# Kernel tuning notes

Measured on AMD Instinct MI355X. Metric: run time of the kernel, lower is better.

Reference implementation:

```python
import jax, jax.numpy as jnp
import numpy as np

B, T, N, F, D, E = 8, 256, 118, 3, 128, 372
G = B * T  # number of graphs after flattening batch*time


def _gcn(x, src, dst, W, b):
    # x: [G, N, Fin] -> PyG GCNConv: X' = D^-1/2 (A+I) D^-1/2 (X W) + b
    h = x @ W  # [G, N, Fout]
    deg = jnp.ones((N,), h.dtype).at[dst].add(1.0)  # in-degree + self loop
    inv = deg ** -0.5
    norm = inv[src] * inv[dst]  # [E]
    agg = h * (1.0 / deg)[None, :, None]  # self-loop term: inv[i]*inv[i] = 1/deg
    agg = agg.at[:, dst].add(h[:, src] * norm[None, :, None])
    return agg + b


def _lstm_layer(x, Wih, Whh, bih, bhh):
    # x: [B, T, I]; PyTorch gate order i, f, g, o
    Bb, H = x.shape[0], Whh.shape[1]
    h0 = jnp.zeros((Bb, H), x.dtype)
    c0 = jnp.zeros((Bb, H), x.dtype)

    def step(carry, xt):
        h, c = carry
        gates = xt @ Wih.T + h @ Whh.T + bih + bhh
        i, f, g, o = jnp.split(gates, 4, axis=-1)
        c = jax.nn.sigmoid(f) * c + jax.nn.sigmoid(i) * jnp.tanh(g)
        h = jax.nn.sigmoid(o) * jnp.tanh(c)
        return (h, c), h

    _, ys = jax.lax.scan(step, (h0, c0), jnp.swapaxes(x, 0, 1))
    return jnp.swapaxes(ys, 0, 1)


def setup_inputs() -> dict:
    key = jax.random.key(0)
    ks = jax.random.split(key, 24)
    s = 0.05

    def rn(i, shape):
        return jax.random.normal(ks[i], shape, jnp.float32) * s

    return {
        "snapshot_sequence": jax.random.normal(ks[0], (B, T, N, F), jnp.float32),
        "edge_index": jax.random.randint(ks[1], (2, E), 0, N, dtype=jnp.int64),
        "scale": jnp.ones((F,), jnp.float32),
        "shift": jnp.zeros((F,), jnp.float32),
        "W1": rn(2, (F, D)), "b1": jnp.zeros((D,), jnp.float32),
        "W2": rn(3, (D, D)), "b2": jnp.zeros((D,), jnp.float32),
        "W3": rn(4, (D, D)), "b3": jnp.zeros((D,), jnp.float32),
        "Wih0": rn(5, (4 * D, D)), "Whh0": rn(6, (4 * D, D)),
        "bih0": jnp.zeros((4 * D,), jnp.float32), "bhh0": jnp.zeros((4 * D,), jnp.float32),
        "Wih1": rn(7, (4 * D, D)), "Whh1": rn(8, (4 * D, D)),
        "bih1": jnp.zeros((4 * D,), jnp.float32), "bhh1": jnp.zeros((4 * D,), jnp.float32),
        "hW1": rn(9, (D, 128)), "hb1": jnp.zeros((128,), jnp.float32),
        "hW2": rn(10, (128, 64)), "hb2": jnp.zeros((64,), jnp.float32),
        "hW3": rn(11, (64, 2)), "hb3": jnp.zeros((2,), jnp.float32),
    }


def reference(snapshot_sequence, edge_index, scale, shift,
              W1, b1, W2, b2, W3, b3,
              Wih0, Whh0, bih0, bhh0, Wih1, Whh1, bih1, bhh1,
              hW1, hb1, hW2, hb2, hW3, hb3):
    src, dst = edge_index[0], edge_index[1]
    x = snapshot_sequence * scale + shift              # FeatureNormalizer
    x = x.reshape(G, N, F)                             # flatten batch*time graphs
    x = jax.nn.silu(_gcn(x, src, dst, W1, b1))         # GCNConv 1 (dropout = eval identity)
    x = jax.nn.silu(_gcn(x, src, dst, W2, b2))         # GCNConv 2
    x = jax.nn.silu(_gcn(x, src, dst, W3, b3))         # GCNConv 3
    emb = x.mean(axis=1)                               # global_mean_pool -> [G, D]
    emb = emb.reshape(B, T, D)
    h = _lstm_layer(emb, Wih0, Whh0, bih0, bhh0)       # 2-layer LSTM (eval: no dropout)
    h = _lstm_layer(h, Wih1, Whh1, bih1, bhh1)
    final = h[:, -1, :]                                # [B, D]
    y = jax.nn.silu(final @ hW1 + hb1)
    y = jax.nn.silu(y @ hW2 + hb2)
    y = y @ hW3 + hb3
    return jax.nn.softplus(y) + 1e-6                   # [B, 2]
```

## Files before the change

### kernel.cpp

```cpp
#include <hip/hip_runtime.h>
#include <math.h>

#define NN 118
#define EE 372
#define GG 2048
#define DD 128
#define TT 256
#define BB 8
#define FD 512

#define XS 136

typedef short bf16x8 __attribute__((ext_vector_type(8)));
typedef float f32x4  __attribute__((ext_vector_type(4)));
typedef _Float16 f16x2 __attribute__((ext_vector_type(2)));

__device__ __forceinline__ float frcp_(float x) { return __builtin_amdgcn_rcpf(x); }
__device__ __forceinline__ float sig_f(float x) { return frcp_(1.0f + __expf(-x)); }
__device__ __forceinline__ float tanh_f(float x) { return 1.0f - 2.0f * frcp_(__expf(2.0f * x) + 1.0f); }
__device__ __forceinline__ float silu_f(float x) { return x * frcp_(1.0f + __expf(-x)); }
__device__ __forceinline__ float siluf_(float x) { return x / (1.0f + expf(-x)); }

__device__ __forceinline__ float fdot2_(unsigned int a, unsigned int b, float c) {
#if defined(__has_builtin) && __has_builtin(__builtin_amdgcn_fdot2)
    return __builtin_amdgcn_fdot2(__builtin_bit_cast(f16x2, a),
                                  __builtin_bit_cast(f16x2, b), c, false);
#else
    f16x2 x = __builtin_bit_cast(f16x2, a), y = __builtin_bit_cast(f16x2, b);
    return c + (float)x[0] * (float)y[0] + (float)x[1] * (float)y[1];
#endif
}

__device__ __forceinline__ void bar_lds() {
    asm volatile("s_waitcnt lgkmcnt(0)\n\ts_barrier" ::: "memory");
}

__device__ __forceinline__ unsigned short f2bf(float x) {
    unsigned int u = __float_as_uint(x);
    unsigned int r = (u + 0x7fffu + ((u >> 16) & 1u)) >> 16;
    return (unsigned short)r;
}
__device__ __forceinline__ float bf2f(unsigned short b) {
    return __uint_as_float(((unsigned int)b) << 16);
}

__global__ void prep_kernel(const int* __restrict__ ei,
                            const float* __restrict__ bih0, const float* __restrict__ bhh0,
                            const float* __restrict__ bih1, const float* __restrict__ bhh1,
                            float* __restrict__ bias0, float* __restrict__ bias1,
                            unsigned short* __restrict__ AbG) {
    __shared__ int sflag;
    __shared__ int ssrc[EE], sdst[EE];
    __shared__ int scount[NN];
    __shared__ float sinv[NN];
    __shared__ float Adense[NN * NN];
    int tid = threadIdx.x;
    if (tid == 0) sflag = 0;
    __syncthreads();
    for (int i = tid; i < 2 * EE; i += blockDim.x)
        if ((i & 1) && ei[i] != 0) atomicOr(&sflag, 1);
    __syncthreads();
    bool m64 = (sflag == 0);
    for (int e = tid; e < EE; e += blockDim.x) {
        int s, d;
        if (m64) { s = ei[2 * e]; d = ei[2 * EE + 2 * e]; }
        else     { s = ei[e];     d = ei[EE + e]; }
        s = min(max(s, 0), NN - 1); d = min(max(d, 0), NN - 1);
        ssrc[e] = s; sdst[e] = d;
    }
    for (int n = tid; n < NN; n += blockDim.x) scount[n] = 0;
    for (int i = tid; i < NN * NN; i += blockDim.x) Adense[i] = 0.0f;
    __syncthreads();
    for (int e = tid; e < EE; e += blockDim.x) atomicAdd(&scount[sdst[e]], 1);
    __syncthreads();
    for (int n = tid; n < NN; n += blockDim.x) {
        float deg = 1.0f + (float)scount[n];
        sinv[n] = rsqrtf(deg);
        Adense[n * NN + n] = 1.0f / deg;
    }
    __syncthreads();
    for (int e = tid; e < EE; e += blockDim.x)
        atomicAdd(&Adense[sdst[e] * NN + ssrc[e]], sinv[ssrc[e]] * sinv[sdst[e]]);
    __syncthreads();
    for (int i = tid; i < 128 * 128; i += blockDim.x) {
        int r = i >> 7, c = i & 127;
        AbG[i] = (r < NN && c < NN) ? f2bf(Adense[r * NN + c]) : (unsigned short)0;
    }
    for (int j = tid; j < FD; j += blockDim.x) {
        bias0[j] = bih0[j] + bhh0[j];
        bias1[j] = bih1[j] + bhh1[j];
    }
}

__global__ void convw_kernel(const float* __restrict__ W, unsigned short* __restrict__ out) {
    int i = blockIdx.x * 512 + threadIdx.x;
    int n = i >> 7, k = i & 127;
    out[i] = f2bf(W[k * DD + n]);
}

__global__ void convh_kernel(const float* __restrict__ W, unsigned int* __restrict__ out) {
    int i = blockIdx.x * 512 + threadIdx.x;
    int d = i & 127;
    int rest = i >> 7;
    int quarter = rest & 3;
    int qg = rest >> 2;
    int q = qg & 15, g = qg >> 4;
    const float* row = W + (size_t)(g * 128 + d) * 128 + quarter * 32;
    float a = row[2 * q], b = row[2 * q + 1];
    unsigned short lo = __builtin_bit_cast(unsigned short, (_Float16)a);
    unsigned short hi = __builtin_bit_cast(unsigned short, (_Float16)b);
    out[i] = (unsigned int)lo | ((unsigned int)hi << 16);
}

__global__ void transpose_kernel(const float* __restrict__ in, float* __restrict__ out) {
    int idx = blockIdx.x * blockDim.x + threadIdx.x;
    int j = idx >> 7, k = idx & 127;
    out[k * FD + j] = in[idx];
}

__device__ __forceinline__ void mm_xw(const unsigned short* __restrict__ xb,
                                      const unsigned short* __restrict__ wtG,
                                      unsigned short* __restrict__ hS, int tid) {
    int lane = tid & 63, w = tid >> 6;
    int lm = lane & 15, lq = lane >> 4;
    int wm = (w & 1) * 64, wn = (w >> 1) * 32;
    f32x4 acc[4][2];
#pragma unroll
    for (int mt = 0; mt < 4; ++mt)
#pragma unroll
        for (int nt = 0; nt < 2; ++nt) acc[mt][nt] = (f32x4){0.f, 0.f, 0.f, 0.f};
#pragma unroll
    for (int kb = 0; kb < 4; ++kb) {
        int ko = kb * 32 + lq * 8;
        bf16x8 b0 = *(const bf16x8*)(wtG + (wn + lm) * 128 + ko);
        bf16x8 b1 = *(const bf16x8*)(wtG + (wn + 16 + lm) * 128 + ko);
#pragma unroll
        for (int mt = 0; mt < 4; ++mt) {
            bf16x8 af = *(const bf16x8*)(xb + (wm + mt * 16 + lm) * XS + ko);
            acc[mt][0] = __builtin_amdgcn_mfma_f32_16x16x32_bf16(af, b0, acc[mt][0], 0, 0, 0);
            acc[mt][1] = __builtin_amdgcn_mfma_f32_16x16x32_bf16(af, b1, acc[mt][1], 0, 0, 0);
        }
    }
#pragma unroll
    for (int mt = 0; mt < 4; ++mt)
#pragma unroll
        for (int nt = 0; nt < 2; ++nt) {
            f32x4 a = acc[mt][nt];
            ushort4 pk;
            pk.x = f2bf(a[0]); pk.y = f2bf(a[1]); pk.z = f2bf(a[2]); pk.w = f2bf(a[3]);
            *(ushort4*)(hS + (wn + nt * 16 + lm) * XS + wm + mt * 16 + lq * 4) = pk;
        }
}

__device__ __forceinline__ void mm_agg(const unsigned short* __restrict__ AbG,
                                       const unsigned short* __restrict__ hS,
                                       unsigned short* __restrict__ xb,
                                       float bn0, float bn1, int tid) {
    int lane = tid & 63, w = tid >> 6;
    int lm = lane & 15, lq = lane >> 4;
    int wm = (w & 1) * 64, wn = (w >> 1) * 32;
    f32x4 acc[4][2];
#pragma unroll
    for (int mt = 0; mt < 4; ++mt)
#pragma unroll
        for (int nt = 0; nt < 2; ++nt) acc[mt][nt] = (f32x4){0.f, 0.f, 0.f, 0.f};
#pragma unroll
    for (int kb = 0; kb < 4; ++kb) {
        int ko = kb * 32 + lq * 8;
        bf16x8 b0 = *(const bf16x8*)(hS + (wn + lm) * XS + ko);
        bf16x8 b1 = *(const bf16x8*)(hS + (wn + 16 + lm) * XS + ko);
#pragma unroll
        for (int mt = 0; mt < 4; ++mt) {
            bf16x8 af = *(const bf16x8*)(AbG + (wm + mt * 16 + lm) * 128 + ko);
            acc[mt][0] = __builtin_amdgcn_mfma_f32_16x16x32_bf16(af, b0, acc[mt][0], 0, 0, 0);
            acc[mt][1] = __builtin_amdgcn_mfma_f32_16x16x32_bf16(af, b1, acc[mt][1], 0, 0, 0);
        }
    }
#pragma unroll
    for (int mt = 0; mt < 4; ++mt)
#pragma unroll
        for (int nt = 0; nt < 2; ++nt) {
            float bn = nt ? bn1 : bn0;
            int col = wn + nt * 16 + lm;
#pragma unroll
            for (int i = 0; i < 4; ++i) {
                float v = silu_f(acc[mt][nt][i] + bn);
                xb[(wm + mt * 16 + lq * 4 + i) * XS + col] = f2bf(v);
            }
        }
}

__global__ __launch_bounds__(512) void gcn_kernel(
    const float* __restrict__ xg, const float* __restrict__ scale, const float* __restrict__ shift,
    const float* __restrict__ W1, const float* __restrict__ b1,
    const float* __restrict__ b2, const float* __restrict__ b3,
    const unsigned short* __restrict__ AbG,
    const unsigned short* __restrict__ Wt2g, const unsigned short* __restrict__ Wt3g,
    float* __restrict__ emb) {
    extern __shared__ char smem[];
    unsigned short* xb = (unsigned short*)smem;
    unsigned short* hS = (unsigned short*)(smem + 34816);
    float* xinL  = (float*)(smem + 69632);
    float* meanS = (float*)(smem + 71056);
    int tid = threadIdx.x;
    int lane = tid & 63, w = tid >> 6;
    int g = blockIdx.x;

    for (int i = tid; i < 2176; i += 512) ((uint4*)hS)[i] = (uint4){0, 0, 0, 0};
    for (int i = tid; i < 170; i += 512) ((uint4*)(xb + NN * XS))[i] = (uint4){0, 0, 0, 0};
    float s0 = scale[0], s1 = scale[1], s2 = scale[2];
    float t0 = shift[0], t1 = shift[1], t2 = shift[2];
    const float* xrow = xg + (size_t)g * (NN * 3);
    for (int i = tid; i < NN * 3; i += 512) {
        int f = i % 3;
        float sc = (f == 0) ? s0 : ((f == 1) ? s1 : s2);
        float sf = (f == 0) ? t0 : ((f == 1) ? t1 : t2);
        xinL[i] = xrow[i] * sc + sf;
    }
    int lm = lane & 15;
    int wn = (w >> 1) * 32;
    int n0 = wn + lm, n1 = wn + 16 + lm;
    float b1a = b1[n0], b1b = b1[n1];
    float b2a = b2[n0], b2b = b2[n1];
    float b3a = b3[n0], b3b = b3[n1];
    int dd = lane * 2;
    float2 w10 = *(const float2*)(W1 + dd);
    float2 w11 = *(const float2*)(W1 + DD + dd);
    float2 w12 = *(const float2*)(W1 + 2 * DD + dd);
    bar_lds();
    for (int k = 0; k < 15; ++k) {
        int n = w + 8 * k;
        if (n >= NN) break;
        float x0 = xinL[n * 3], x1 = xinL[n * 3 + 1], x2 = xinL[n * 3 + 2];
        hS[dd * XS + n]       = f2bf(x0 * w10.x + x1 * w11.x + x2 * w12.x);
        hS[(dd + 1) * XS + n] = f2bf(x0 * w10.y + x1 * w11.y + x2 * w12.y);
    }
    bar_lds();
    mm_agg(AbG, hS, xb, b1a, b1b, tid);
    bar_lds();
    mm_xw(xb, Wt2g, hS, tid);
    bar_lds();
    mm_agg(AbG, hS, xb, b2a, b2b, tid);
    bar_lds();
    mm_xw(xb, Wt3g, hS, tid);
    bar_lds();
    mm_agg(AbG, hS, xb, b3a, b3b, tid);
    bar_lds();
    {
        int d = tid & 127, part = tid >> 7;
        int a0 = part * 30;
        int a1 = (a0 + 30 < NN) ? (a0 + 30) : NN;
        float s = 0.f;
        for (int n = a0; n < a1; ++n) s += bf2f(xb[n * XS + d]);
        meanS[part * 128 + d] = s;
    }
    bar_lds();
    if (tid < 128) {
        float s = meanS[tid] + meanS[128 + tid] + meanS[256 + tid] + meanS[384 + tid];
        emb[(size_t)g * DD + tid] = s * (1.0f / (float)NN);
    }
}

__global__ __launch_bounds__(512) void proj_kernel(const float* __restrict__ src,
                                                   const float* __restrict__ WT,
                                                   const float* __restrict__ bias,
                                                   float* __restrict__ dst) {
    __shared__ __align__(16) float eL[DD];
    int g = blockIdx.x, tid = threadIdx.x;
    if (tid < DD) eL[tid] = src[(size_t)g * DD + tid];
    __syncthreads();
    float acc = bias[tid];
    const float* wt = WT + tid;
#pragma unroll 8
    for (int k = 0; k < DD; ++k) acc += eL[k] * wt[(size_t)k * FD];
    dst[(size_t)g * FD + tid] = acc;
}

__global__ __launch_bounds__(512, 2) void scan_kernel(
    const float* __restrict__ inp,
    const unsigned int* __restrict__ Wc,
    float* __restrict__ hout, int full) {
    __shared__ __align__(16) unsigned short hL[DD];
    __shared__ __align__(16) float sgP[3 * DD * 4];
    int b = blockIdx.x, j = threadIdx.x;
    int d = j & 127, quarter = j >> 7;
    unsigned int wreg[4][16];
#pragma unroll
    for (int g = 0; g < 4; ++g)
#pragma unroll
        for (int q = 0; q < 16; ++q)
            wreg[g][q] = Wc[(((g * 16 + q) << 2) + quarter) * 128 + d];
#pragma unroll
    for (int g = 0; g < 4; ++g)
#pragma unroll
        for (int q = 0; q < 16; ++q)
            asm volatile("" : "+v"(wreg[g][q]));
    if (j < 64) ((unsigned int*)hL)[j] = 0u;
    float creg = 0.f;
    const float* ib = inp + (size_t)b * TT * FD;
    float* hb_ = hout + (size_t)b * (full ? TT * DD : DD);
    float xg0[4], xg1[4];
    if (quarter == 0) {
#pragma unroll
        for (int g = 0; g < 4; ++g) { xg0[g] = ib[g * DD + d]; xg1[g] = ib[FD + g * DD + d]; }
    }
    bar_lds();
    for (int t = 0; t < TT; ++t) {
        float xg2[4];
        if (quarter == 0) {
            bool more = (t + 2 < TT);
#pragma unroll
            for (int g = 0; g < 4; ++g)
                xg2[g] = more ? ib[(t + 2) * FD + g * DD + d] : 0.f;
        }
        const uint4* h4 = (const uint4*)(hL + quarter * 32);
        float a0 = 0.f, a1 = 0.f, a2 = 0.f, a3 = 0.f;
#pragma unroll
        for (int c = 0; c < 4; ++c) {
            uint4 hv = h4[c];
            a0 = fdot2_(wreg[0][4 * c + 0], hv.x, a0);
            a1 = fdot2_(wreg[1][4 * c + 0], hv.x, a1);
            a2 = fdot2_(wreg[2][4 * c + 0], hv.x, a2);
            a3 = fdot2_(wreg[3][4 * c + 0], hv.x, a3);
            a0 = fdot2_(wreg[0][4 * c + 1], hv.y, a0);
            a1 = fdot2_(wreg[1][4 * c + 1], hv.y, a1);
            a2 = fdot2_(wreg[2][4 * c + 1], hv.y, a2);
            a3 = fdot2_(wreg[3][4 * c + 1], hv.y, a3);
            a0 = fdot2_(wreg[0][4 * c + 2], hv.z, a0);
            a1 = fdot2_(wreg[1][4 * c + 2], hv.z, a1);
            a2 = fdot2_(wreg[2][4 * c + 2], hv.z, a2);
            a3 = fdot2_(wreg[3][4 * c + 2], hv.z, a3);
            a0 = fdot2_(wreg[0][4 * c + 3], hv.w, a0);
            a1 = fdot2_(wreg[1][4 * c + 3], hv.w, a1);
            a2 = fdot2_(wreg[2][4 * c + 3], hv.w, a2);
            a3 = fdot2_(wreg[3][4 * c + 3], hv.w, a3);
        }
        if (quarter != 0)
            *(float4*)(sgP + ((quarter - 1) * DD + d) * 4) = make_float4(a0, a1, a2, a3);
        bar_lds();
        if (quarter == 0) {
            float4 p1 = *(const float4*)(sgP + d * 4);
            float4 p2 = *(const float4*)(sgP + (DD + d) * 4);
            float4 p3 = *(const float4*)(sgP + (2 * DD + d) * 4);
            float iv = sig_f(a0 + p1.x + p2.x + p3.x + xg0[0]);
            float fv = sig_f(a1 + p1.y + p2.y + p3.y + xg0[1]);
            float gv = tanh_f(a2 + p1.z + p2.z + p3.z + xg0[2]);
            float ov = sig_f(a3 + p1.w + p2.w + p3.w + xg0[3]);
            float cn = fv * creg + iv * gv;
            creg = cn;
            float hn = ov * tanh_f(cn);
            ((_Float16*)hL)[d] = (_Float16)hn;
            if (full) hb_[t * DD + d] = hn;
            else if (t == TT - 1) hb_[d] = hn;
#pragma unroll
            for (int g = 0; g < 4; ++g) { xg0[g] = xg1[g]; xg1[g] = xg2[g]; }
        }
        bar_lds();
    }
}

__global__ void head_kernel(const float* __restrict__ hfin,
                            const float* __restrict__ hW1, const float* __restrict__ hb1,
                            const float* __restrict__ hW2, const float* __restrict__ hb2,
                            const float* __restrict__ hW3, const float* __restrict__ hb3,
                            float* __restrict__ out) {
    __shared__ float fh[BB * DD];
    __shared__ float y1[BB * DD];
    __shared__ float y2[BB * 64];
    int tid = threadIdx.x;
    for (int i = tid; i < BB * DD; i += 256) fh[i] = hfin[i];
    __syncthreads();
    for (int i = tid; i < BB * DD; i += 256) {
        int bb = i >> 7, jj = i & 127;
        float acc = hb1[jj];
        for (int k = 0; k < DD; ++k) acc += fh[(bb << 7) + k] * hW1[(k << 7) + jj];
        y1[i] = siluf_(acc);
    }
    __syncthreads();
    for (int i = tid; i < BB * 64; i += 256) {
        int bb = i >> 6, jj = i & 63;
        float acc = hb2[jj];
        for (int k = 0; k < DD; ++k) acc += y1[(bb << 7) + k] * hW2[(k << 6) + jj];
        y2[i] = siluf_(acc);
    }
    __syncthreads();
    if (tid < BB * 2) {
        int bb = tid >> 1, m = tid & 1;
        float acc = hb3[m];
        for (int k = 0; k < 64; ++k) acc += y2[(bb << 6) + k] * hW3[k * 2 + m];
        float sp = fmaxf(acc, 0.f) + log1pf(expf(-fabsf(acc)));
        out[tid] = sp + 1e-6f;
    }
}

extern "C" void kernel_launch(void* const* d_in, const int* in_sizes, int n_in,
                              void* d_out, int out_size, void* d_ws, size_t ws_size,
                              hipStream_t stream) {
    const float* snap  = (const float*)d_in[0];
    const int*   edges = (const int*)d_in[1];
    const float* scale = (const float*)d_in[2];
    const float* shift = (const float*)d_in[3];
    const float* W1 = (const float*)d_in[4];
    const float* b1 = (const float*)d_in[5];
    const float* W2 = (const float*)d_in[6];
    const float* b2 = (const float*)d_in[7];
    const float* W3 = (const float*)d_in[8];
    const float* b3 = (const float*)d_in[9];
    const float* Wih0 = (const float*)d_in[10];
    const float* Whh0 = (const float*)d_in[11];
    const float* bih0 = (const float*)d_in[12];
    const float* bhh0 = (const float*)d_in[13];
    const float* Wih1 = (const float*)d_in[14];
    const float* Whh1 = (const float*)d_in[15];
    const float* bih1 = (const float*)d_in[16];
    const float* bhh1 = (const float*)d_in[17];
    const float* hW1 = (const float*)d_in[18];
    const float* hb1 = (const float*)d_in[19];
    const float* hW2 = (const float*)d_in[20];
    const float* hb2 = (const float*)d_in[21];
    const float* hW3 = (const float*)d_in[22];
    const float* hb3 = (const float*)d_in[23];

    float* ws = (float*)d_ws;
    float* bias0 = ws + 0;
    float* bias1 = ws + 512;
    unsigned short* AbG  = (unsigned short*)(ws + 1024);
    unsigned short* Wt2g = (unsigned short*)(ws + 9216);
    unsigned short* Wt3g = (unsigned short*)(ws + 17408);
    float* WT0 = ws + 25600;
    float* WT1 = ws + 91136;
    unsigned int* Wc0 = (unsigned int*)(ws + 156672);
    unsigned int* Wc1 = (unsigned int*)(ws + 189440);
    float* emb   = ws + 222208;
    float* inp   = ws + 484352;
    float* h0seq = ws + 1532928;
    float* hfin  = ws + 1795072;

    const int smem_gcn = 73104;
    hipFuncSetAttribute((const void*)gcn_kernel,
                        hipFuncAttributeMaxDynamicSharedMemorySize, smem_gcn);

    prep_kernel<<<1, 256, 0, stream>>>(edges, bih0, bhh0, bih1, bhh1,
                                       bias0, bias1, AbG);
    convw_kernel<<<32, 512, 0, stream>>>(W2, Wt2g);
    convw_kernel<<<32, 512, 0, stream>>>(W3, Wt3g);
    convh_kernel<<<64, 512, 0, stream>>>(Whh0, Wc0);
    convh_kernel<<<64, 512, 0, stream>>>(Whh1, Wc1);
    transpose_kernel<<<128, 512, 0, stream>>>(Wih0, WT0);
    transpose_kernel<<<128, 512, 0, stream>>>(Wih1, WT1);
    gcn_kernel<<<GG, 512, smem_gcn, stream>>>(snap, scale, shift, W1, b1, b2, b3,
                                              AbG, Wt2g, Wt3g, emb);
    proj_kernel<<<GG, 512, 0, stream>>>(emb, WT0, bias0, inp);
    scan_kernel<<<BB, 512, 0, stream>>>(inp, Wc0, h0seq, 1);
    proj_kernel<<<GG, 512, 0, stream>>>(h0seq, WT1, bias1, inp);
    scan_kernel<<<BB, 512, 0, stream>>>(inp, Wc1, hfin, 0);
    head_kernel<<<1, 256, 0, stream>>>(hfin, hW1, hb1, hW2, hb2, hW3, hb3, (float*)d_out);
}
```

Before: 627.1 us.

## Process two graphs per GCN block with larger per-wave MFMA tiles

The GCN kernel now handles two graphs per 512-thread block, four waves per graph. Each wave computes a 64x64 output tile instead of 64x32, so every loaded A fragment feeds four MFMAs instead of two, and the grid is halved. The aim is more operand reuse and less per-block setup and barrier overhead. In exchange, LDS use roughly doubles to about 142KB, likely limiting each CU to one block, and the extra accumulators raise register pressure, which may reduce latency hiding.

```diff
diff --git a/kernel.cpp b/kernel.cpp
--- a/kernel.cpp
+++ b/kernel.cpp
@@ -10,6 +10,7 @@
 #define FD 512
 
 #define XS 136
+#define MS 264
 
 typedef short bf16x8 __attribute__((ext_vector_type(8)));
 typedef float f32x4  __attribute__((ext_vector_type(4)));
@@ -118,79 +119,81 @@
     out[k * FD + j] = in[idx];
 }
 
-__device__ __forceinline__ void mm_xw(const unsigned short* __restrict__ xb,
-                                      const unsigned short* __restrict__ wtG,
-                                      unsigned short* __restrict__ hS, int tid) {
-    int lane = tid & 63, w = tid >> 6;
-    int lm = lane & 15, lq = lane >> 4;
-    int wm = (w & 1) * 64, wn = (w >> 1) * 32;
-    f32x4 acc[4][2];
+__device__ __forceinline__ void mm_agg2(const unsigned short* __restrict__ AbG,
+                                        const unsigned short* __restrict__ hS2,
+                                        unsigned short* __restrict__ xb2,
+                                        const float* __restrict__ bias,
+                                        int gr, int wm, int wn, int lm, int lq) {
+    f32x4 acc[4][4];
 #pragma unroll
     for (int mt = 0; mt < 4; ++mt)
 #pragma unroll
-        for (int nt = 0; nt < 2; ++nt) acc[mt][nt] = (f32x4){0.f, 0.f, 0.f, 0.f};
+        for (int nt = 0; nt < 4; ++nt) acc[mt][nt] = (f32x4){0.f, 0.f, 0.f, 0.f};
 #pragma unroll
     for (int kb = 0; kb < 4; ++kb) {
         int ko = kb * 32 + lq * 8;
-        bf16x8 b0 = *(const bf16x8*)(wtG + (wn + lm) * 128 + ko);
-        bf16x8 b1 = *(const bf16x8*)(wtG + (wn + 16 + lm) * 128 + ko);
+        bf16x8 bfr[4];
+#pragma unroll
+        for (int nt = 0; nt < 4; ++nt)
+            bfr[nt] = *(const bf16x8*)(hS2 + (wn + nt * 16 + lm) * MS + gr * 128 + ko);
 #pragma unroll
         for (int mt = 0; mt < 4; ++mt) {
-            bf16x8 af = *(const bf16x8*)(xb + (wm + mt * 16 + lm) * XS + ko);
-            acc[mt][0] = __builtin_amdgcn_mfma_f32_16x16x32_bf16(af, b0, acc[mt][0], 0, 0, 0);
-            acc[mt][1] = __builtin_amdgcn_mfma_f32_16x16x32_bf16(af, b1, acc[mt][1], 0, 0, 0);
-        }
-    }
+            bf16x8 af = *(const bf16x8*)(AbG + (wm + mt * 16 + lm) * 128 + ko);
+#pragma unroll
+            for (int nt = 0; nt < 4; ++nt)
+                acc[mt][nt] = __builtin_amdgcn_mfma_f32_16x16x32_bf16(af, bfr[nt], acc[mt][nt], 0, 0, 0);
+        }
+    }
+#pragma unroll
+    for (int nt = 0; nt < 4; ++nt) {
+        float bn = bias[wn + nt * 16 + lm];
+        int col = wn + nt * 16 + lm;
+#pragma unroll
+        for (int mt = 0; mt < 4; ++mt)
+#pragma unroll
+            for (int i = 0; i < 4; ++i) {
+                float v = silu_f(acc[mt][nt][i] + bn);
+                xb2[(gr * 128 + wm + mt * 16 + lq * 4 + i) * XS + col] = f2bf(v);
+            }
+    }
+}
+
+__device__ __forceinline__ void mm_xw2(const unsigned short* __restrict__ xb2,
+                                       const unsigned short* __restrict__ WtG,
+                                       unsigned short* __restrict__ hS2,
+                                       int gr, int wm, int wn, int lm, int lq) {
+    f32x4 acc[4][4];
 #pragma unroll
     for (int mt = 0; mt < 4; ++mt)
 #pragma unroll
-        for (int nt = 0; nt < 2; ++nt) {
+        for (int nt = 0; nt < 4; ++nt) acc[mt][nt] = (f32x4){0.f, 0.f, 0.f, 0.f};
+#pragma unroll
+    for (int kb = 0; kb < 4; ++kb) {
+        int ko = kb * 32 + lq * 8;
+        bf16x8 bfr[4];
+#pragma unroll
+        for (int nt = 0; nt < 4; ++nt)
+            bfr[nt] = *(const bf16x8*)(WtG + (wn + nt * 16 + lm) * 128 + ko);
+#pragma unroll
+        for (int mt = 0; mt < 4; ++mt) {
+            bf16x8 af = *(const bf16x8*)(xb2 + (gr * 128 + wm + mt * 16 + lm) * XS + ko);
+#pragma unroll
+            for (int nt = 0; nt < 4; ++nt)
+                acc[mt][nt] = __builtin_amdgcn_mfma_f32_16x16x32_bf16(af, bfr[nt], acc[mt][nt], 0, 0, 0);
+        }
+    }
+#pragma unroll
+    for (int nt = 0; nt < 4; ++nt)
+#pragma unroll
+        for (int mt = 0; mt < 4; ++mt) {
             f32x4 a = acc[mt][nt];
             ushort4 pk;
             pk.x = f2bf(a[0]); pk.y = f2bf(a[1]); pk.z = f2bf(a[2]); pk.w = f2bf(a[3]);
-            *(ushort4*)(hS + (wn + nt * 16 + lm) * XS + wm + mt * 16 + lq * 4) = pk;
-        }
-}
-
-__device__ __forceinline__ void mm_agg(const unsigned short* __restrict__ AbG,
-                                       const unsigned short* __restrict__ hS,
-                                       unsigned short* __restrict__ xb,
-                                       float bn0, float bn1, int tid) {
-    int lane = tid & 63, w = tid >> 6;
-    int lm = lane & 15, lq = lane >> 4;
-    int wm = (w & 1) * 64, wn = (w >> 1) * 32;
-    f32x4 acc[4][2];
-#pragma unroll
-    for (int mt = 0; mt < 4; ++mt)
-#pragma unroll
-        for (int nt = 0; nt < 2; ++nt) acc[mt][nt] = (f32x4){0.f, 0.f, 0.f, 0.f};
-#pragma unroll
-    for (int kb = 0; kb < 4; ++kb) {
-        int ko = kb * 32 + lq * 8;
-        bf16x8 b0 = *(const bf16x8*)(hS + (wn + lm) * XS + ko);
-        bf16x8 b1 = *(const bf16x8*)(hS + (wn + 16 + lm) * XS + ko);
-#pragma unroll
-        for (int mt = 0; mt < 4; ++mt) {
-            bf16x8 af = *(const bf16x8*)(AbG + (wm + mt * 16 + lm) * 128 + ko);
-            acc[mt][0] = __builtin_amdgcn_mfma_f32_16x16x32_bf16(af, b0, acc[mt][0], 0, 0, 0);
-            acc[mt][1] = __builtin_amdgcn_mfma_f32_16x16x32_bf16(af, b1, acc[mt][1], 0, 0, 0);
-        }
-    }
-#pragma unroll
-    for (int mt = 0; mt < 4; ++mt)
-#pragma unroll
-        for (int nt = 0; nt < 2; ++nt) {
-            float bn = nt ? bn1 : bn0;
-            int col = wn + nt * 16 + lm;
-#pragma unroll
-            for (int i = 0; i < 4; ++i) {
-                float v = silu_f(acc[mt][nt][i] + bn);
-                xb[(wm + mt * 16 + lq * 4 + i) * XS + col] = f2bf(v);
-            }
-        }
-}
-
-__global__ __launch_bounds__(512) void gcn_kernel(
+            *(ushort4*)(hS2 + (wn + nt * 16 + lm) * MS + gr * 128 + wm + mt * 16 + lq * 4) = pk;
+        }
+}
+
+__global__ __launch_bounds__(512, 2) void gcn_kernel(
     const float* __restrict__ xg, const float* __restrict__ scale, const float* __restrict__ shift,
     const float* __restrict__ W1, const float* __restrict__ b1,
     const float* __restrict__ b2, const float* __restrict__ b3,
@@ -198,66 +201,72 @@
     const unsigned short* __restrict__ Wt2g, const unsigned short* __restrict__ Wt3g,
     float* __restrict__ emb) {
     extern __shared__ char smem[];
-    unsigned short* xb = (unsigned short*)smem;
-    unsigned short* hS = (unsigned short*)(smem + 34816);
-    float* xinL  = (float*)(smem + 69632);
-    float* meanS = (float*)(smem + 71056);
+    unsigned short* xb2 = (unsigned short*)smem;
+    unsigned short* hS2 = (unsigned short*)(smem + 69632);
+    float* xin2  = (float*)(smem + 137216);
+    float* meanS = (float*)(smem + 140048);
     int tid = threadIdx.x;
     int lane = tid & 63, w = tid >> 6;
-    int g = blockIdx.x;
-
-    for (int i = tid; i < 2176; i += 512) ((uint4*)hS)[i] = (uint4){0, 0, 0, 0};
-    for (int i = tid; i < 170; i += 512) ((uint4*)(xb + NN * XS))[i] = (uint4){0, 0, 0, 0};
+    int gr = w >> 2;
+    int wl = w & 3;
+    int lm = lane & 15, lq = lane >> 4;
+    int wm = (wl & 1) * 64, wn = (wl >> 1) * 64;
+    int g0 = blockIdx.x * 2;
+
+    for (int i = tid; i < 4224; i += 512) ((uint4*)hS2)[i] = (uint4){0, 0, 0, 0};
+    for (int i = tid; i < 2 * 10 * 64; i += 512) {
+        int grr = i >= 640;
+        int ii = i - grr * 640;
+        int r = grr * 128 + NN + (ii >> 6), c = (ii & 63) * 2;
+        *(unsigned int*)(xb2 + r * XS + c) = 0u;
+    }
     float s0 = scale[0], s1 = scale[1], s2 = scale[2];
     float t0 = shift[0], t1 = shift[1], t2 = shift[2];
-    const float* xrow = xg + (size_t)g * (NN * 3);
-    for (int i = tid; i < NN * 3; i += 512) {
-        int f = i % 3;
+    for (int i = tid; i < 2 * NN * 3; i += 512) {
+        int gi = (i >= NN * 3) ? 1 : 0;
+        int idx = i - gi * (NN * 3);
+        int f = idx % 3;
         float sc = (f == 0) ? s0 : ((f == 1) ? s1 : s2);
         float sf = (f == 0) ? t0 : ((f == 1) ? t1 : t2);
-        xinL[i] = xrow[i] * sc + sf;
-    }
-    int lm = lane & 15;
-    int wn = (w >> 1) * 32;
-    int n0 = wn + lm, n1 = wn + 16 + lm;
-    float b1a = b1[n0], b1b = b1[n1];
-    float b2a = b2[n0], b2b = b2[n1];
-    float b3a = b3[n0], b3b = b3[n1];
+        xin2[gi * 354 + idx] = xg[(size_t)(g0 + gi) * (NN * 3) + idx] * sc + sf;
+    }
     int dd = lane * 2;
     float2 w10 = *(const float2*)(W1 + dd);
     float2 w11 = *(const float2*)(W1 + DD + dd);
     float2 w12 = *(const float2*)(W1 + 2 * DD + dd);
     bar_lds();
-    for (int k = 0; k < 15; ++k) {
-        int n = w + 8 * k;
+    const float* xin = xin2 + gr * 354;
+    for (int k = 0; k < 30; ++k) {
+        int n = wl + 4 * k;
         if (n >= NN) break;
-        float x0 = xinL[n * 3], x1 = xinL[n * 3 + 1], x2 = xinL[n * 3 + 2];
-        hS[dd * XS + n]       = f2bf(x0 * w10.x + x1 * w11.x + x2 * w12.x);
-        hS[(dd + 1) * XS + n] = f2bf(x0 * w10.y + x1 * w11.y + x2 * w12.y);
-    }
-    bar_lds();
-    mm_agg(AbG, hS, xb, b1a, b1b, tid);
-    bar_lds();
-    mm_xw(xb, Wt2g, hS, tid);
-    bar_lds();
-    mm_agg(AbG, hS, xb, b2a, b2b, tid);
-    bar_lds();
-    mm_xw(xb, Wt3g, hS, tid);
-    bar_lds();
-    mm_agg(AbG, hS, xb, b3a, b3b, tid);
+        float x0 = xin[n * 3], x1 = xin[n * 3 + 1], x2 = xin[n * 3 + 2];
+        hS2[dd * MS + gr * 128 + n]       = f2bf(x0 * w10.x + x1 * w11.x + x2 * w12.x);
+        hS2[(dd + 1) * MS + gr * 128 + n] = f2bf(x0 * w10.y + x1 * w11.y + x2 * w12.y);
+    }
+    bar_lds();
+    mm_agg2(AbG, hS2, xb2, b1, gr, wm, wn, lm, lq);
+    bar_lds();
+    mm_xw2(xb2, Wt2g, hS2, gr, wm, wn, lm, lq);
+    bar_lds();
+    mm_agg2(AbG, hS2, xb2, b2, gr, wm, wn, lm, lq);
+    bar_lds();
+    mm_xw2(xb2, Wt3g, hS2, gr, wm, wn, lm, lq);
+    bar_lds();
+    mm_agg2(AbG, hS2, xb2, b3, gr, wm, wn, lm, lq);
     bar_lds();
     {
-        int d = tid & 127, part = tid >> 7;
-        int a0 = part * 30;
-        int a1 = (a0 + 30 < NN) ? (a0 + 30) : NN;
+        int grr = tid >> 8, t2 = tid & 255;
+        int part = t2 >> 7, d = t2 & 127;
+        int a0 = part * 59, a1 = a0 + 59;
         float s = 0.f;
-        for (int n = a0; n < a1; ++n) s += bf2f(xb[n * XS + d]);
-        meanS[part * 128 + d] = s;
-    }
-    bar_lds();
-    if (tid < 128) {
-        float s = meanS[tid] + meanS[128 + tid] + meanS[256 + tid] + meanS[384 + tid];
-        emb[(size_t)g * DD + tid] = s * (1.0f / (float)NN);
+        for (int n = a0; n < a1; ++n) s += bf2f(xb2[(grr * 128 + n) * XS + d]);
+        meanS[grr * 256 + part * 128 + d] = s;
+    }
+    bar_lds();
+    if (tid < 256) {
+        int grr = tid >> 7, d = tid & 127;
+        float s = meanS[grr * 256 + d] + meanS[grr * 256 + 128 + d];
+        emb[(size_t)(g0 + grr) * DD + d] = s * (1.0f / (float)NN);
     }
 }
 
@@ -436,7 +445,7 @@
     float* h0seq = ws + 1532928;
     float* hfin  = ws + 1795072;
 
-    const int smem_gcn = 73104;
+    const int smem_gcn = 142096;
     hipFuncSetAttribute((const void*)gcn_kernel,
                         hipFuncAttributeMaxDynamicSharedMemorySize, smem_gcn);
 
@@ -448,8 +457,8 @@
     convh_kernel<<<64, 512, 0, stream>>>(Whh1, Wc1);
     transpose_kernel<<<128, 512, 0, stream>>>(Wih0, WT0);
     transpose_kernel<<<128, 512, 0, stream>>>(Wih1, WT1);
-    gcn_kernel<<<GG, 512, smem_gcn, stream>>>(snap, scale, shift, W1, b1, b2, b3,
-                                              AbG, Wt2g, Wt3g, emb);
+    gcn_kernel<<<GG / 2, 512, smem_gcn, stream>>>(snap, scale, shift, W1, b1, b2, b3,
+                                                  AbG, Wt2g, Wt3g, emb);
     proj_kernel<<<GG, 512, 0, stream>>>(emb, WT0, bias0, inp);
     scan_kernel<<<BB, 512, 0, stream>>>(inp, Wc0, h0seq, 1);
     proj_kernel<<<GG, 512, 0, stream>>>(h0seq, WT1, bias1, inp);
```

Result: faster. 604.0 us (-3.7%).
